# Kernel tuning notes

Hardware: AMD Instinct MI355X
Metric: run time of the kernel (lower is better)

Reference implementation:

```python
import jax, jax.numpy as jnp
import numpy as np
from jax import lax

H = 64            # hidden size
NUM_LAYERS = 3
EMBED_LEN = 128
B, T = 256, 2048


def _lstm_layer(x, Wih, Whh, bih, bhh):
    """x: [B, T, in]; returns full hidden sequence [B, T, H].
    PyTorch gate order: i, f, g, o."""
    Bn = x.shape[0]
    b = bih + bhh  # [4H]
    # Precompute input contribution for all timesteps: [T, B, 4H]
    xg = jnp.einsum('bti,gi->tbg', x, Wih) + b
    h0 = jnp.zeros((Bn, H), x.dtype)
    c0 = jnp.zeros((Bn, H), x.dtype)

    def step(carry, xg_t):
        h, c = carry
        gates = xg_t + h @ Whh.T  # [B, 4H]
        i, f, g, o = jnp.split(gates, 4, axis=-1)
        i = jax.nn.sigmoid(i)
        f = jax.nn.sigmoid(f)
        g = jnp.tanh(g)
        o = jax.nn.sigmoid(o)
        c = f * c + i * g
        h = o * jnp.tanh(c)
        return (h, c), h

    (_, _), hs = lax.scan(step, (h0, c0), xg)  # hs: [T, B, H]
    return jnp.swapaxes(hs, 0, 1)              # [B, T, H]


def setup_inputs() -> dict:
    key = jax.random.key(0)
    ks = jax.random.split(key, 20)
    k = 1.0 / np.sqrt(H)  # PyTorch default init bound

    def u(kk, shape):
        return jax.random.uniform(kk, shape, jnp.float32, -k, k)

    inp = {"x": jax.random.normal(ks[0], (B, 1, T), jnp.float32)}
    in_sizes = [1, H, H]
    idx = 1
    for l in range(NUM_LAYERS):
        inp[f"Wih{l}"] = u(ks[idx], (4 * H, in_sizes[l])); idx += 1
        inp[f"Whh{l}"] = u(ks[idx], (4 * H, H)); idx += 1
        inp[f"bih{l}"] = u(ks[idx], (4 * H,)); idx += 1
        inp[f"bhh{l}"] = u(ks[idx], (4 * H,)); idx += 1
    inp["fcW"] = u(ks[idx], (EMBED_LEN, H)); idx += 1
    inp["fcb"] = u(ks[idx], (EMBED_LEN,))
    return inp


def reference(x, Wih0, Whh0, bih0, bhh0,
              Wih1, Whh1, bih1, bhh1,
              Wih2, Whh2, bih2, bhh2,
              fcW, fcb):
    # forward: transpose [B,1,T] -> [B,T,1]
    h = jnp.swapaxes(x, 1, 2)
    h = _lstm_layer(h, Wih0, Whh0, bih0, bhh0)
    h = _lstm_layer(h, Wih1, Whh1, bih1, bhh1)
    h = _lstm_layer(h, Wih2, Whh2, bih2, bhh2)
    last = h[:, -1, :]              # [B, H]
    return last @ fcW.T + fcb       # [B, EMBED_LEN]
```

## Files before the change

kernel.cpp:

```cpp
#include <hip/hip_runtime.h>

#define T_LEN 2048
#define HID 64
#define EMB 128
#define WD 16
#define NWIN (T_LEN / WD)
#define NPH (NWIN + 4)

typedef _Float16 half2_t __attribute__((ext_vector_type(2)));
typedef unsigned uint4v __attribute__((ext_vector_type(4)));

#if __has_builtin(__builtin_amdgcn_exp2f)
#define EXP2F(x) __builtin_amdgcn_exp2f(x)
#else
#define EXP2F(x) exp2f(x)
#endif
#if __has_builtin(__builtin_amdgcn_rcpf)
#define RCPF(x) __builtin_amdgcn_rcpf(x)
#else
#define RCPF(x) (1.0f / (x))
#endif

#define LOG2E 1.4426950408889634f

__device__ __forceinline__ float fdot2(unsigned a, unsigned b, float c) {
    return __builtin_amdgcn_fdot2(__builtin_bit_cast(half2_t, a),
                                  __builtin_bit_cast(half2_t, b), c, false);
}

__device__ __forceinline__ float dotrow(const uint4v* w, const uint4v* g, float init) {
    float a0 = init, a1 = 0.f, a2 = 0.f, a3 = 0.f;
    #pragma unroll
    for (int q = 0; q < 8; ++q) {
        a0 = fdot2(w[q][0], g[q][0], a0);
        a1 = fdot2(w[q][1], g[q][1], a1);
        a2 = fdot2(w[q][2], g[q][2], a2);
        a3 = fdot2(w[q][3], g[q][3], a3);
    }
    return (a0 + a1) + (a2 + a3);
}

__device__ __forceinline__ uint4v pack8(float4 a, float4 b, float s) {
    half2_t h0{(_Float16)(a.x * s), (_Float16)(a.y * s)};
    half2_t h1{(_Float16)(a.z * s), (_Float16)(a.w * s)};
    half2_t h2{(_Float16)(b.x * s), (_Float16)(b.y * s)};
    half2_t h3{(_Float16)(b.z * s), (_Float16)(b.w * s)};
    uint4v q;
    q[0] = __builtin_bit_cast(unsigned, h0);
    q[1] = __builtin_bit_cast(unsigned, h1);
    q[2] = __builtin_bit_cast(unsigned, h2);
    q[3] = __builtin_bit_cast(unsigned, h3);
    return q;
}

__device__ __forceinline__ void cvt8(const float* __restrict__ Wp, float s, uint4v* dst) {
    const float4* p = reinterpret_cast<const float4*>(Wp);
    #pragma unroll
    for (int k = 0; k < 8; ++k) dst[k] = pack8(p[2 * k], p[2 * k + 1], s);
}

__global__ __launch_bounds__(512)
__attribute__((amdgpu_waves_per_eu(2, 2)))
void lstm3_fused(
    const float* __restrict__ x,
    const float* __restrict__ Wih0, const float* __restrict__ Whh0,
    const float* __restrict__ bih0, const float* __restrict__ bhh0,
    const float* __restrict__ Wih1, const float* __restrict__ Whh1,
    const float* __restrict__ bih1, const float* __restrict__ bhh1,
    const float* __restrict__ Wih2, const float* __restrict__ Whh2,
    const float* __restrict__ bih2, const float* __restrict__ bhh2,
    const float* __restrict__ fcW,  const float* __restrict__ fcb,
    float* __restrict__ out)
{
    const int b   = blockIdx.x;
    const int tid = threadIdx.x;
    const int wv  = tid >> 6;
    const int L   = tid & 63;

    __shared__ __align__(16) _Float16 h0ring[2 * WD][HID];
    __shared__ __align__(16) _Float16 h1ring[2 * WD][HID];
    __shared__ __align__(16) _Float16 h2ring[2][HID];
    __shared__ float p1buf[2][WD][4][HID];
    __shared__ float p2buf[2][WD][4][HID];
    __shared__ __align__(16) float xs[T_LEN];

    {
        const float4* xg4 = reinterpret_cast<const float4*>(x + b * T_LEN);
        reinterpret_cast<float4*>(xs)[tid] = xg4[tid];
        reinterpret_cast<unsigned*>(h0ring)[tid] = 0u;
        reinterpret_cast<unsigned*>(h0ring)[tid + 512] = 0u;
        reinterpret_cast<unsigned*>(h1ring)[tid] = 0u;
        reinterpret_cast<unsigned*>(h1ring)[tid + 512] = 0u;
        if (tid < 64) reinterpret_cast<unsigned*>(h2ring)[tid] = 0u;
    }

    const float sI = -LOG2E, sF = -LOG2E, sG = -2.f * LOG2E, sO = -LOG2E;
    const float scl[4] = {sI, sF, sG, sO};

    uint4v w[4][8];
    float bias4[4] = {0.f, 0.f, 0.f, 0.f};
    float wx4[4]   = {0.f, 0.f, 0.f, 0.f};

    if (wv < 3) {
        const float* Wh = (wv == 0) ? Whh0 : (wv == 1) ? Whh1 : Whh2;
        const float* bi = (wv == 0) ? bih0 : (wv == 1) ? bih1 : bih2;
        const float* bh = (wv == 0) ? bhh0 : (wv == 1) ? bhh1 : bhh2;
        #pragma unroll
        for (int c = 0; c < 4; ++c) {
            cvt8(Wh + (c * 64 + L) * 64, scl[c], w[c]);
            bias4[c] = (bi[c * 64 + L] + bh[c * 64 + L]) * scl[c];
        }
        if (wv == 0) {
            #pragma unroll
            for (int c = 0; c < 4; ++c) wx4[c] = Wih0[c * 64 + L] * scl[c];
        }
    } else if (wv == 4) {
        cvt8(Wih1 + (  0 + L) * 64, sI, w[0]);
    } else if (wv == 5) {
        cvt8(Wih1 + ( 64 + L) * 64, sF, w[0]);
    } else if (wv == 6) {
        cvt8(Wih1 + (128 + L) * 64, sG, w[0]);
    } else if (wv == 3) {
        cvt8(Wih1 + (192 + L) * 64, sO, w[0]);
        cvt8(Wih2 + (  0 + L) * 64, sI, w[1]);
    } else {
        cvt8(Wih2 + ( 64 + L) * 64, sF, w[0]);
        cvt8(Wih2 + (128 + L) * 64, sG, w[1]);
        cvt8(Wih2 + (192 + L) * 64, sO, w[2]);
    }

    float cst = 0.f;
    __syncthreads();

    for (int ph = 0; ph < NPH; ++ph) {
        const int par = ph & 1;

        if (wv == 0) {
            if (ph < NWIN) {
                _Float16* cur = &h0ring[par * WD][0];
                const _Float16* prv = &h0ring[(par ^ 1) * WD][0];
                const int tb = ph * WD;
                #pragma unroll 8
                for (int j = 0; j < WD; ++j) {
                    const uint4v* hp = reinterpret_cast<const uint4v*>(
                        (j == 0) ? (prv + (WD - 1) * HID) : (cur + (j - 1) * HID));
                    uint4v g[8];
                    #pragma unroll
                    for (int k = 0; k < 8; ++k) g[k] = hp[k];
                    float xv = xs[tb + j];
                    float d0 = dotrow(w[0], g, fmaf(wx4[0], xv, bias4[0]));
                    float d1 = dotrow(w[1], g, fmaf(wx4[1], xv, bias4[1]));
                    float d2 = dotrow(w[2], g, fmaf(wx4[2], xv, bias4[2]));
                    float d3 = dotrow(w[3], g, fmaf(wx4[3], xv, bias4[3]));
                    float ai = RCPF(1.f + EXP2F(d0));
                    float af = RCPF(1.f + EXP2F(d1));
                    float ag = fmaf(2.f, RCPF(1.f + EXP2F(d2)), -1.f);
                    float ao = RCPF(1.f + EXP2F(d3));
                    cst = fmaf(af, cst, ai * ag);
                    float tc = fmaf(2.f, RCPF(1.f + EXP2F(-2.f * LOG2E * cst)), -1.f);
                    cur[j * HID + L] = (_Float16)(ao * tc);
                }
            }
        } else if (wv == 1) {
            if (ph >= 2 && ph < NWIN + 2) {
                _Float16* cur = &h1ring[par * WD][0];
                const _Float16* prv = &h1ring[(par ^ 1) * WD][0];
                const float (*pb)[4][HID] = p1buf[par];
                #pragma unroll 8
                for (int j = 0; j < WD; ++j) {
                    const uint4v* hp = reinterpret_cast<const uint4v*>(
                        (j == 0) ? (prv + (WD - 1) * HID) : (cur + (j - 1) * HID));
                    uint4v g[8];
                    #pragma unroll
                    for (int k = 0; k < 8; ++k) g[k] = hp[k];
                    float d0 = dotrow(w[0], g, bias4[0] + pb[j][0][L]);
                    float d1 = dotrow(w[1], g, bias4[1] + pb[j][1][L]);
                    float d2 = dotrow(w[2], g, bias4[2] + pb[j][2][L]);
                    float d3 = dotrow(w[3], g, bias4[3] + pb[j][3][L]);
                    float ai = RCPF(1.f + EXP2F(d0));
                    float af = RCPF(1.f + EXP2F(d1));
                    float ag = fmaf(2.f, RCPF(1.f + EXP2F(d2)), -1.f);
                    float ao = RCPF(1.f + EXP2F(d3));
                    cst = fmaf(af, cst, ai * ag);
                    float tc = fmaf(2.f, RCPF(1.f + EXP2F(-2.f * LOG2E * cst)), -1.f);
                    cur[j * HID + L] = (_Float16)(ao * tc);
                }
            }
        } else if (wv == 2) {
            if (ph >= 4) {
                const float (*pb)[4][HID] = p2buf[par];
                #pragma unroll 8
                for (int j = 0; j < WD; ++j) {
                    const uint4v* hp = reinterpret_cast<const uint4v*>(
                        &h2ring[(j & 1) ^ 1][0]);
                    uint4v g[8];
                    #pragma unroll
                    for (int k = 0; k < 8; ++k) g[k] = hp[k];
                    float d0 = dotrow(w[0], g, bias4[0] + pb[j][0][L]);
                    float d1 = dotrow(w[1], g, bias4[1] + pb[j][1][L]);
                    float d2 = dotrow(w[2], g, bias4[2] + pb[j][2][L]);
                    float d3 = dotrow(w[3], g, bias4[3] + pb[j][3][L]);
                    float ai = RCPF(1.f + EXP2F(d0));
                    float af = RCPF(1.f + EXP2F(d1));
                    float ag = fmaf(2.f, RCPF(1.f + EXP2F(d2)), -1.f);
                    float ao = RCPF(1.f + EXP2F(d3));
                    cst = fmaf(af, cst, ai * ag);
                    float tc = fmaf(2.f, RCPF(1.f + EXP2F(-2.f * LOG2E * cst)), -1.f);
                    h2ring[j & 1][L] = (_Float16)(ao * tc);
                }
            }
        } else {
            const bool p1act = (ph >= 1 && ph < NWIN + 1);
            const bool p2act = (ph >= 3 && ph < NWIN + 3);
            if (wv == 4 || wv == 5 || wv == 6) {
                if (p1act) {
                    const _Float16* hw = &h0ring[(par ^ 1) * WD][0];
                    float (*po)[4][HID] = p1buf[par ^ 1];
                    const int c0 = wv - 4;
                    #pragma unroll 8
                    for (int j = 0; j < WD; ++j) {
                        const uint4v* hp = reinterpret_cast<const uint4v*>(hw + j * HID);
                        uint4v g[8];
                        #pragma unroll
                        for (int k = 0; k < 8; ++k) g[k] = hp[k];
                        po[j][c0][L] = dotrow(w[0], g, 0.f);
                    }
                }
            } else if (wv == 3) {
                if (p1act) {
                    const _Float16* hw = &h0ring[(par ^ 1) * WD][0];
                    float (*po)[4][HID] = p1buf[par ^ 1];
                    #pragma unroll 8
                    for (int j = 0; j < WD; ++j) {
                        const uint4v* hp = reinterpret_cast<const uint4v*>(hw + j * HID);
                        uint4v g[8];
                        #pragma unroll
                        for (int k = 0; k < 8; ++k) g[k] = hp[k];
                        po[j][3][L] = dotrow(w[0], g, 0.f);
                    }
                }
                if (p2act) {
                    const _Float16* hw = &h1ring[(par ^ 1) * WD][0];
                    float (*po)[4][HID] = p2buf[par ^ 1];
                    #pragma unroll 8
                    for (int j = 0; j < WD; ++j) {
                        const uint4v* hp = reinterpret_cast<const uint4v*>(hw + j * HID);
                        uint4v g[8];
                        #pragma unroll
                        for (int k = 0; k < 8; ++k) g[k] = hp[k];
                        po[j][0][L] = dotrow(w[1], g, 0.f);
                    }
                }
            } else {
                if (p2act) {
                    const _Float16* hw = &h1ring[(par ^ 1) * WD][0];
                    float (*po)[4][HID] = p2buf[par ^ 1];
                    #pragma unroll 4
                    for (int j = 0; j < WD; ++j) {
                        const uint4v* hp = reinterpret_cast<const uint4v*>(hw + j * HID);
                        uint4v g[8];
                        #pragma unroll
                        for (int k = 0; k < 8; ++k) g[k] = hp[k];
                        po[j][1][L] = dotrow(w[0], g, 0.f);
                        po[j][2][L] = dotrow(w[1], g, 0.f);
                        po[j][3][L] = dotrow(w[2], g, 0.f);
                    }
                }
            }
        }

        __syncthreads();
    }

    if (tid < EMB) {
        float acc = fcb[tid];
        const _Float16* hf = &h2ring[1][0];
        const float4* W4 = reinterpret_cast<const float4*>(fcW + tid * HID);
        #pragma unroll
        for (int k = 0; k < 16; ++k) {
            float4 wv4 = W4[k];
            acc = fmaf(wv4.x, (float)hf[4 * k + 0], acc);
            acc = fmaf(wv4.y, (float)hf[4 * k + 1], acc);
            acc = fmaf(wv4.z, (float)hf[4 * k + 2], acc);
            acc = fmaf(wv4.w, (float)hf[4 * k + 3], acc);
        }
        out[b * EMB + tid] = acc;
    }
}

extern "C" void kernel_launch(void* const* d_in, const int* in_sizes, int n_in,
                              void* d_out, int out_size, void* d_ws, size_t ws_size,
                              hipStream_t stream) {
    const float* x    = (const float*)d_in[0];
    const float* Wih0 = (const float*)d_in[1];
    const float* Whh0 = (const float*)d_in[2];
    const float* bih0 = (const float*)d_in[3];
    const float* bhh0 = (const float*)d_in[4];
    const float* Wih1 = (const float*)d_in[5];
    const float* Whh1 = (const float*)d_in[6];
    const float* bih1 = (const float*)d_in[7];
    const float* bhh1 = (const float*)d_in[8];
    const float* Wih2 = (const float*)d_in[9];
    const float* Whh2 = (const float*)d_in[10];
    const float* bih2 = (const float*)d_in[11];
    const float* bhh2 = (const float*)d_in[12];
    const float* fcW  = (const float*)d_in[13];
    const float* fcb  = (const float*)d_in[14];
    float* out = (float*)d_out;

    lstm3_fused<<<dim3(256), dim3(512), 0, stream>>>(
        x, Wih0, Whh0, bih0, bhh0,
        Wih1, Whh1, bih1, bhh1,
        Wih2, Whh2, bih2, bhh2,
        fcW, fcb, out);
}
```

Measured before the change: 1.085 ms.

## Replace per-phase block barrier with per-wave LDS flag dependencies and halve window

```diff
diff --git a/kernel.cpp b/kernel.cpp
--- a/kernel.cpp
+++ b/kernel.cpp
@@ -3,7 +3,7 @@
 #define T_LEN 2048
 #define HID 64
 #define EMB 128
-#define WD 16
+#define WD 8
 #define NWIN (T_LEN / WD)
 #define NPH (NWIN + 4)
 
@@ -57,6 +57,10 @@
     const float4* p = reinterpret_cast<const float4*>(Wp);
     #pragma unroll
     for (int k = 0; k < 8; ++k) dst[k] = pack8(p[2 * k], p[2 * k + 1], s);
+}
+
+__device__ __forceinline__ int ldf(int* f) {
+    return __hip_atomic_load(f, __ATOMIC_RELAXED, __HIP_MEMORY_SCOPE_WORKGROUP);
 }
 
 __global__ __launch_bounds__(512)
@@ -83,15 +87,15 @@
     __shared__ float p1buf[2][WD][4][HID];
     __shared__ float p2buf[2][WD][4][HID];
     __shared__ __align__(16) float xs[T_LEN];
+    __shared__ int flags[8];
 
     {
         const float4* xg4 = reinterpret_cast<const float4*>(x + b * T_LEN);
         reinterpret_cast<float4*>(xs)[tid] = xg4[tid];
-        reinterpret_cast<unsigned*>(h0ring)[tid] = 0u;
-        reinterpret_cast<unsigned*>(h0ring)[tid + 512] = 0u;
-        reinterpret_cast<unsigned*>(h1ring)[tid] = 0u;
-        reinterpret_cast<unsigned*>(h1ring)[tid + 512] = 0u;
+        reinterpret_cast<unsigned*>(h0ring)[tid & 511] = 0u;
+        reinterpret_cast<unsigned*>(h1ring)[tid & 511] = 0u;
         if (tid < 64) reinterpret_cast<unsigned*>(h2ring)[tid] = 0u;
+        if (tid < 8) flags[tid] = 0;
     }
 
     const float sI = -LOG2E, sF = -LOG2E, sG = -2.f * LOG2E, sO = -LOG2E;
@@ -135,12 +139,36 @@
     for (int ph = 0; ph < NPH; ++ph) {
         const int par = ph & 1;
 
+        {
+            bool ok;
+            do {
+                if (wv == 0)
+                    ok = (ldf(&flags[3]) >= ph) & (ldf(&flags[4]) >= ph)
+                       & (ldf(&flags[5]) >= ph) & (ldf(&flags[6]) >= ph);
+                else if (wv == 1)
+                    ok = (ldf(&flags[3]) >= ph) & (ldf(&flags[4]) >= ph)
+                       & (ldf(&flags[5]) >= ph) & (ldf(&flags[6]) >= ph)
+                       & (ldf(&flags[7]) >= ph);
+                else if (wv == 2)
+                    ok = (ldf(&flags[3]) >= ph) & (ldf(&flags[7]) >= ph);
+                else if (wv == 3)
+                    ok = (ldf(&flags[0]) >= ph) & (ldf(&flags[1]) >= ph)
+                       & (ldf(&flags[2]) >= ph);
+                else if (wv == 7)
+                    ok = (ldf(&flags[1]) >= ph) & (ldf(&flags[2]) >= ph);
+                else
+                    ok = (ldf(&flags[0]) >= ph) & (ldf(&flags[1]) >= ph);
+                if (!ok) __builtin_amdgcn_s_sleep(1);
+            } while (!ok);
+            __builtin_amdgcn_fence(__ATOMIC_ACQUIRE, "workgroup");
+        }
+
         if (wv == 0) {
             if (ph < NWIN) {
                 _Float16* cur = &h0ring[par * WD][0];
                 const _Float16* prv = &h0ring[(par ^ 1) * WD][0];
                 const int tb = ph * WD;
-                #pragma unroll 8
+                #pragma unroll
                 for (int j = 0; j < WD; ++j) {
                     const uint4v* hp = reinterpret_cast<const uint4v*>(
                         (j == 0) ? (prv + (WD - 1) * HID) : (cur + (j - 1) * HID));
@@ -166,7 +194,7 @@
                 _Float16* cur = &h1ring[par * WD][0];
                 const _Float16* prv = &h1ring[(par ^ 1) * WD][0];
                 const float (*pb)[4][HID] = p1buf[par];
-                #pragma unroll 8
+                #pragma unroll
                 for (int j = 0; j < WD; ++j) {
                     const uint4v* hp = reinterpret_cast<const uint4v*>(
                         (j == 0) ? (prv + (WD - 1) * HID) : (cur + (j - 1) * HID));
@@ -189,7 +217,7 @@
         } else if (wv == 2) {
             if (ph >= 4) {
                 const float (*pb)[4][HID] = p2buf[par];
-                #pragma unroll 8
+                #pragma unroll
                 for (int j = 0; j < WD; ++j) {
                     const uint4v* hp = reinterpret_cast<const uint4v*>(
                         &h2ring[(j & 1) ^ 1][0]);
@@ -217,7 +245,7 @@
                     const _Float16* hw = &h0ring[(par ^ 1) * WD][0];
                     float (*po)[4][HID] = p1buf[par ^ 1];
                     const int c0 = wv - 4;
-                    #pragma unroll 8
+                    #pragma unroll
                     for (int j = 0; j < WD; ++j) {
                         const uint4v* hp = reinterpret_cast<const uint4v*>(hw + j * HID);
                         uint4v g[8];
@@ -230,7 +258,7 @@
                 if (p1act) {
                     const _Float16* hw = &h0ring[(par ^ 1) * WD][0];
                     float (*po)[4][HID] = p1buf[par ^ 1];
-                    #pragma unroll 8
+                    #pragma unroll
                     for (int j = 0; j < WD; ++j) {
                         const uint4v* hp = reinterpret_cast<const uint4v*>(hw + j * HID);
                         uint4v g[8];
@@ -242,7 +270,7 @@
                 if (p2act) {
                     const _Float16* hw = &h1ring[(par ^ 1) * WD][0];
                     float (*po)[4][HID] = p2buf[par ^ 1];
-                    #pragma unroll 8
+                    #pragma unroll
                     for (int j = 0; j < WD; ++j) {
                         const uint4v* hp = reinterpret_cast<const uint4v*>(hw + j * HID);
                         uint4v g[8];
@@ -255,7 +283,7 @@
                 if (p2act) {
                     const _Float16* hw = &h1ring[(par ^ 1) * WD][0];
                     float (*po)[4][HID] = p2buf[par ^ 1];
-                    #pragma unroll 4
+                    #pragma unroll
                     for (int j = 0; j < WD; ++j) {
                         const uint4v* hp = reinterpret_cast<const uint4v*>(hw + j * HID);
                         uint4v g[8];
@@ -269,8 +297,13 @@
             }
         }
 
-        __syncthreads();
-    }
+        __builtin_amdgcn_fence(__ATOMIC_RELEASE, "workgroup");
+        if ((tid & 63) == 0)
+            __hip_atomic_store(&flags[wv], ph + 1, __ATOMIC_RELAXED,
+                               __HIP_MEMORY_SCOPE_WORKGROUP);
+    }
+
+    __syncthreads();
 
     if (tid < EMB) {
         float acc = fcb[tid];
```

After: 1.027 ms. 5.4% less time.

## Grow block to 12 waves and split input projections across more waves

Applied to the files above, without the earlier changes.

```diff
diff --git a/kernel.cpp b/kernel.cpp
--- a/kernel.cpp
+++ b/kernel.cpp
@@ -3,7 +3,7 @@
 #define T_LEN 2048
 #define HID 64
 #define EMB 128
-#define WD 16
+#define WD 8
 #define NWIN (T_LEN / WD)
 #define NPH (NWIN + 4)
 
@@ -38,6 +38,18 @@
         a3 = fdot2(w[q][3], g[q][3], a3);
     }
     return (a0 + a1) + (a2 + a3);
+}
+
+__device__ __forceinline__ float dot16h(const uint4v* w, const uint4v* g) {
+    float e = 0.f, o = 0.f;
+    #pragma unroll
+    for (int q = 0; q < 4; ++q) {
+        e = fdot2(w[q][0], g[q][0], e);
+        o = fdot2(w[q][1], g[q][1], o);
+        e = fdot2(w[q][2], g[q][2], e);
+        o = fdot2(w[q][3], g[q][3], o);
+    }
+    return e + o;
 }
 
 __device__ __forceinline__ uint4v pack8(float4 a, float4 b, float s) {
@@ -58,9 +70,14 @@
     #pragma unroll
     for (int k = 0; k < 8; ++k) dst[k] = pack8(p[2 * k], p[2 * k + 1], s);
 }
-
-__global__ __launch_bounds__(512)
-__attribute__((amdgpu_waves_per_eu(2, 2)))
+__device__ __forceinline__ void cvt4(const float* __restrict__ Wp, float s, uint4v* dst) {
+    const float4* p = reinterpret_cast<const float4*>(Wp);
+    #pragma unroll
+    for (int k = 0; k < 4; ++k) dst[k] = pack8(p[2 * k], p[2 * k + 1], s);
+}
+
+__global__ __launch_bounds__(768)
+__attribute__((amdgpu_waves_per_eu(3, 3)))
 void lstm3_fused(
     const float* __restrict__ x,
     const float* __restrict__ Wih0, const float* __restrict__ Whh0,
@@ -80,18 +97,21 @@
     __shared__ __align__(16) _Float16 h0ring[2 * WD][HID];
     __shared__ __align__(16) _Float16 h1ring[2 * WD][HID];
     __shared__ __align__(16) _Float16 h2ring[2][HID];
-    __shared__ float p1buf[2][WD][4][HID];
+    __shared__ float p1a[2][WD][4][HID];
+    __shared__ float p1b[2][WD][4][HID];
     __shared__ float p2buf[2][WD][4][HID];
     __shared__ __align__(16) float xs[T_LEN];
 
     {
         const float4* xg4 = reinterpret_cast<const float4*>(x + b * T_LEN);
-        reinterpret_cast<float4*>(xs)[tid] = xg4[tid];
-        reinterpret_cast<unsigned*>(h0ring)[tid] = 0u;
-        reinterpret_cast<unsigned*>(h0ring)[tid + 512] = 0u;
-        reinterpret_cast<unsigned*>(h1ring)[tid] = 0u;
-        reinterpret_cast<unsigned*>(h1ring)[tid + 512] = 0u;
+        if (tid < 512) {
+            reinterpret_cast<float4*>(xs)[tid] = xg4[tid];
+            reinterpret_cast<unsigned*>(h0ring)[tid] = 0u;
+            reinterpret_cast<unsigned*>(h1ring)[tid] = 0u;
+        }
         if (tid < 64) reinterpret_cast<unsigned*>(h2ring)[tid] = 0u;
+        float* pz = &p1b[0][0][0][0];
+        for (int i = tid; i < 2 * WD * 4 * HID; i += 768) pz[i] = 0.f;
     }
 
     const float sI = -LOG2E, sF = -LOG2E, sG = -2.f * LOG2E, sO = -LOG2E;
@@ -114,19 +134,20 @@
             #pragma unroll
             for (int c = 0; c < 4; ++c) wx4[c] = Wih0[c * 64 + L] * scl[c];
         }
-    } else if (wv == 4) {
-        cvt8(Wih1 + (  0 + L) * 64, sI, w[0]);
-    } else if (wv == 5) {
-        cvt8(Wih1 + ( 64 + L) * 64, sF, w[0]);
-    } else if (wv == 6) {
-        cvt8(Wih1 + (128 + L) * 64, sG, w[0]);
+    } else if (wv == 4 || wv == 5 || wv == 6) {
+        const int c = wv - 4;
+        cvt4(Wih1 + (c * 64 + L) * 64, scl[c], w[0]);
+    } else if (wv == 8 || wv == 9 || wv == 10) {
+        const int c = wv - 8;
+        cvt4(Wih1 + (c * 64 + L) * 64 + 32, scl[c], w[0]);
     } else if (wv == 3) {
         cvt8(Wih1 + (192 + L) * 64, sO, w[0]);
         cvt8(Wih2 + (  0 + L) * 64, sI, w[1]);
-    } else {
+    } else if (wv == 7) {
         cvt8(Wih2 + ( 64 + L) * 64, sF, w[0]);
         cvt8(Wih2 + (128 + L) * 64, sG, w[1]);
-        cvt8(Wih2 + (192 + L) * 64, sO, w[2]);
+    } else {
+        cvt8(Wih2 + (192 + L) * 64, sO, w[0]);
     }
 
     float cst = 0.f;
@@ -140,7 +161,7 @@
                 _Float16* cur = &h0ring[par * WD][0];
                 const _Float16* prv = &h0ring[(par ^ 1) * WD][0];
                 const int tb = ph * WD;
-                #pragma unroll 8
+                #pragma unroll
                 for (int j = 0; j < WD; ++j) {
                     const uint4v* hp = reinterpret_cast<const uint4v*>(
                         (j == 0) ? (prv + (WD - 1) * HID) : (cur + (j - 1) * HID));
@@ -165,18 +186,19 @@
             if (ph >= 2 && ph < NWIN + 2) {
                 _Float16* cur = &h1ring[par * WD][0];
                 const _Float16* prv = &h1ring[(par ^ 1) * WD][0];
-                const float (*pb)[4][HID] = p1buf[par];
-                #pragma unroll 8
+                const float (*pa)[4][HID] = p1a[par];
+                const float (*pb)[4][HID] = p1b[par];
+                #pragma unroll
                 for (int j = 0; j < WD; ++j) {
                     const uint4v* hp = reinterpret_cast<const uint4v*>(
                         (j == 0) ? (prv + (WD - 1) * HID) : (cur + (j - 1) * HID));
                     uint4v g[8];
                     #pragma unroll
                     for (int k = 0; k < 8; ++k) g[k] = hp[k];
-                    float d0 = dotrow(w[0], g, bias4[0] + pb[j][0][L]);
-                    float d1 = dotrow(w[1], g, bias4[1] + pb[j][1][L]);
-                    float d2 = dotrow(w[2], g, bias4[2] + pb[j][2][L]);
-                    float d3 = dotrow(w[3], g, bias4[3] + pb[j][3][L]);
+                    float d0 = dotrow(w[0], g, bias4[0] + pa[j][0][L] + pb[j][0][L]);
+                    float d1 = dotrow(w[1], g, bias4[1] + pa[j][1][L] + pb[j][1][L]);
+                    float d2 = dotrow(w[2], g, bias4[2] + pa[j][2][L] + pb[j][2][L]);
+                    float d3 = dotrow(w[3], g, bias4[3] + pa[j][3][L] + pb[j][3][L]);
                     float ai = RCPF(1.f + EXP2F(d0));
                     float af = RCPF(1.f + EXP2F(d1));
                     float ag = fmaf(2.f, RCPF(1.f + EXP2F(d2)), -1.f);
@@ -189,7 +211,7 @@
         } else if (wv == 2) {
             if (ph >= 4) {
                 const float (*pb)[4][HID] = p2buf[par];
-                #pragma unroll 8
+                #pragma unroll
                 for (int j = 0; j < WD; ++j) {
                     const uint4v* hp = reinterpret_cast<const uint4v*>(
                         &h2ring[(j & 1) ^ 1][0]);
@@ -215,22 +237,36 @@
             if (wv == 4 || wv == 5 || wv == 6) {
                 if (p1act) {
                     const _Float16* hw = &h0ring[(par ^ 1) * WD][0];
-                    float (*po)[4][HID] = p1buf[par ^ 1];
-                    const int c0 = wv - 4;
-                    #pragma unroll 8
-                    for (int j = 0; j < WD; ++j) {
-                        const uint4v* hp = reinterpret_cast<const uint4v*>(hw + j * HID);
-                        uint4v g[8];
-                        #pragma unroll
-                        for (int k = 0; k < 8; ++k) g[k] = hp[k];
-                        po[j][c0][L] = dotrow(w[0], g, 0.f);
+                    float (*po)[4][HID] = p1a[par ^ 1];
+                    const int c = wv - 4;
+                    #pragma unroll
+                    for (int j = 0; j < WD; ++j) {
+                        const uint4v* hp = reinterpret_cast<const uint4v*>(hw + j * HID);
+                        uint4v g[4];
+                        #pragma unroll
+                        for (int k = 0; k < 4; ++k) g[k] = hp[k];
+                        po[j][c][L] = dot16h(w[0], g);
+                    }
+                }
+            } else if (wv == 8 || wv == 9 || wv == 10) {
+                if (p1act) {
+                    const _Float16* hw = &h0ring[(par ^ 1) * WD][0];
+                    float (*po)[4][HID] = p1b[par ^ 1];
+                    const int c = wv - 8;
+                    #pragma unroll
+                    for (int j = 0; j < WD; ++j) {
+                        const uint4v* hp = reinterpret_cast<const uint4v*>(hw + j * HID) + 4;
+                        uint4v g[4];
+                        #pragma unroll
+                        for (int k = 0; k < 4; ++k) g[k] = hp[k];
+                        po[j][c][L] = dot16h(w[0], g);
                     }
                 }
             } else if (wv == 3) {
                 if (p1act) {
                     const _Float16* hw = &h0ring[(par ^ 1) * WD][0];
-                    float (*po)[4][HID] = p1buf[par ^ 1];
-                    #pragma unroll 8
+                    float (*po)[4][HID] = p1a[par ^ 1];
+                    #pragma unroll
                     for (int j = 0; j < WD; ++j) {
                         const uint4v* hp = reinterpret_cast<const uint4v*>(hw + j * HID);
                         uint4v g[8];
@@ -242,28 +278,40 @@
                 if (p2act) {
                     const _Float16* hw = &h1ring[(par ^ 1) * WD][0];
                     float (*po)[4][HID] = p2buf[par ^ 1];
-                    #pragma unroll 8
+                    #pragma unroll
                     for (int j = 0; j < WD; ++j) {
                         const uint4v* hp = reinterpret_cast<const uint4v*>(hw + j * HID);
                         uint4v g[8];
                         #pragma unroll
                         for (int k = 0; k < 8; ++k) g[k] = hp[k];
                         po[j][0][L] = dotrow(w[1], g, 0.f);
+                    }
+                }
+            } else if (wv == 7) {
+                if (p2act) {
+                    const _Float16* hw = &h1ring[(par ^ 1) * WD][0];
+                    float (*po)[4][HID] = p2buf[par ^ 1];
+                    #pragma unroll
+                    for (int j = 0; j < WD; ++j) {
+                        const uint4v* hp = reinterpret_cast<const uint4v*>(hw + j * HID);
+                        uint4v g[8];
+                        #pragma unroll
+                        for (int k = 0; k < 8; ++k) g[k] = hp[k];
+                        po[j][1][L] = dotrow(w[0], g, 0.f);
+                        po[j][2][L] = dotrow(w[1], g, 0.f);
                     }
                 }
             } else {
                 if (p2act) {
                     const _Float16* hw = &h1ring[(par ^ 1) * WD][0];
                     float (*po)[4][HID] = p2buf[par ^ 1];
-                    #pragma unroll 4
+                    #pragma unroll
                     for (int j = 0; j < WD; ++j) {
                         const uint4v* hp = reinterpret_cast<const uint4v*>(hw + j * HID);
                         uint4v g[8];
                         #pragma unroll
                         for (int k = 0; k < 8; ++k) g[k] = hp[k];
-                        po[j][1][L] = dotrow(w[0], g, 0.f);
-                        po[j][2][L] = dotrow(w[1], g, 0.f);
-                        po[j][3][L] = dotrow(w[2], g, 0.f);
+                        po[j][3][L] = dotrow(w[0], g, 0.f);
                     }
                 }
             }
@@ -308,7 +356,7 @@
     const float* fcb  = (const float*)d_in[14];
     float* out = (float*)d_out;
 
-    lstm3_fused<<<dim3(256), dim3(512), 0, stream>>>(
+    lstm3_fused<<<dim3(256), dim3(768), 0, stream>>>(
         x, Wih0, Whh0, bih0, bhh0,
         Wih1, Whh1, bih1, bhh1,
         Wih2, Whh2, bih2, bhh2,
```

New measurement: 2.058 ms. 1.9x slower.

## Interleave gate preactivation buffers and halve the pipeline window width

Applied to the files above, without the earlier changes.

```diff
diff --git a/kernel.cpp b/kernel.cpp
--- a/kernel.cpp
+++ b/kernel.cpp
@@ -3,7 +3,7 @@
 #define T_LEN 2048
 #define HID 64
 #define EMB 128
-#define WD 16
+#define WD 8
 #define NWIN (T_LEN / WD)
 #define NPH (NWIN + 4)
 
@@ -80,17 +80,15 @@
     __shared__ __align__(16) _Float16 h0ring[2 * WD][HID];
     __shared__ __align__(16) _Float16 h1ring[2 * WD][HID];
     __shared__ __align__(16) _Float16 h2ring[2][HID];
-    __shared__ float p1buf[2][WD][4][HID];
-    __shared__ float p2buf[2][WD][4][HID];
+    __shared__ __align__(16) float p1buf[2][WD][4 * HID];
+    __shared__ __align__(16) float p2buf[2][WD][4 * HID];
     __shared__ __align__(16) float xs[T_LEN];
 
     {
         const float4* xg4 = reinterpret_cast<const float4*>(x + b * T_LEN);
         reinterpret_cast<float4*>(xs)[tid] = xg4[tid];
         reinterpret_cast<unsigned*>(h0ring)[tid] = 0u;
-        reinterpret_cast<unsigned*>(h0ring)[tid + 512] = 0u;
         reinterpret_cast<unsigned*>(h1ring)[tid] = 0u;
-        reinterpret_cast<unsigned*>(h1ring)[tid + 512] = 0u;
         if (tid < 64) reinterpret_cast<unsigned*>(h2ring)[tid] = 0u;
     }
 
@@ -140,7 +138,7 @@
                 _Float16* cur = &h0ring[par * WD][0];
                 const _Float16* prv = &h0ring[(par ^ 1) * WD][0];
                 const int tb = ph * WD;
-                #pragma unroll 8
+                #pragma unroll
                 for (int j = 0; j < WD; ++j) {
                     const uint4v* hp = reinterpret_cast<const uint4v*>(
                         (j == 0) ? (prv + (WD - 1) * HID) : (cur + (j - 1) * HID));
@@ -165,18 +163,19 @@
             if (ph >= 2 && ph < NWIN + 2) {
                 _Float16* cur = &h1ring[par * WD][0];
                 const _Float16* prv = &h1ring[(par ^ 1) * WD][0];
-                const float (*pb)[4][HID] = p1buf[par];
-                #pragma unroll 8
+                const float (*pb)[4 * HID] = p1buf[par];
+                #pragma unroll
                 for (int j = 0; j < WD; ++j) {
                     const uint4v* hp = reinterpret_cast<const uint4v*>(
                         (j == 0) ? (prv + (WD - 1) * HID) : (cur + (j - 1) * HID));
                     uint4v g[8];
                     #pragma unroll
                     for (int k = 0; k < 8; ++k) g[k] = hp[k];
-                    float d0 = dotrow(w[0], g, bias4[0] + pb[j][0][L]);
-                    float d1 = dotrow(w[1], g, bias4[1] + pb[j][1][L]);
-                    float d2 = dotrow(w[2], g, bias4[2] + pb[j][2][L]);
-                    float d3 = dotrow(w[3], g, bias4[3] + pb[j][3][L]);
+                    float4 pv = *reinterpret_cast<const float4*>(&pb[j][L * 4]);
+                    float d0 = dotrow(w[0], g, bias4[0] + pv.w);
+                    float d1 = dotrow(w[1], g, bias4[1] + pv.x);
+                    float d2 = dotrow(w[2], g, bias4[2] + pv.y);
+                    float d3 = dotrow(w[3], g, bias4[3] + pv.z);
                     float ai = RCPF(1.f + EXP2F(d0));
                     float af = RCPF(1.f + EXP2F(d1));
                     float ag = fmaf(2.f, RCPF(1.f + EXP2F(d2)), -1.f);
@@ -188,18 +187,19 @@
             }
         } else if (wv == 2) {
             if (ph >= 4) {
-                const float (*pb)[4][HID] = p2buf[par];
-                #pragma unroll 8
+                const float (*pb)[4 * HID] = p2buf[par];
+                #pragma unroll
                 for (int j = 0; j < WD; ++j) {
                     const uint4v* hp = reinterpret_cast<const uint4v*>(
                         &h2ring[(j & 1) ^ 1][0]);
                     uint4v g[8];
                     #pragma unroll
                     for (int k = 0; k < 8; ++k) g[k] = hp[k];
-                    float d0 = dotrow(w[0], g, bias4[0] + pb[j][0][L]);
-                    float d1 = dotrow(w[1], g, bias4[1] + pb[j][1][L]);
-                    float d2 = dotrow(w[2], g, bias4[2] + pb[j][2][L]);
-                    float d3 = dotrow(w[3], g, bias4[3] + pb[j][3][L]);
+                    float4 pv = *reinterpret_cast<const float4*>(&pb[j][L * 4]);
+                    float d0 = dotrow(w[0], g, bias4[0] + pv.w);
+                    float d1 = dotrow(w[1], g, bias4[1] + pv.x);
+                    float d2 = dotrow(w[2], g, bias4[2] + pv.y);
+                    float d3 = dotrow(w[3], g, bias4[3] + pv.z);
                     float ai = RCPF(1.f + EXP2F(d0));
                     float af = RCPF(1.f + EXP2F(d1));
                     float ag = fmaf(2.f, RCPF(1.f + EXP2F(d2)), -1.f);
@@ -215,55 +215,58 @@
             if (wv == 4 || wv == 5 || wv == 6) {
                 if (p1act) {
                     const _Float16* hw = &h0ring[(par ^ 1) * WD][0];
-                    float (*po)[4][HID] = p1buf[par ^ 1];
-                    const int c0 = wv - 4;
-                    #pragma unroll 8
+                    float (*po)[4 * HID] = p1buf[par ^ 1];
+                    const int pos = (wv == 4) ? 3 : (wv - 5);
+                    #pragma unroll
                     for (int j = 0; j < WD; ++j) {
                         const uint4v* hp = reinterpret_cast<const uint4v*>(hw + j * HID);
                         uint4v g[8];
                         #pragma unroll
                         for (int k = 0; k < 8; ++k) g[k] = hp[k];
-                        po[j][c0][L] = dotrow(w[0], g, 0.f);
+                        po[j][L * 4 + pos] = dotrow(w[0], g, 0.f);
                     }
                 }
             } else if (wv == 3) {
                 if (p1act) {
                     const _Float16* hw = &h0ring[(par ^ 1) * WD][0];
-                    float (*po)[4][HID] = p1buf[par ^ 1];
-                    #pragma unroll 8
+                    float (*po)[4 * HID] = p1buf[par ^ 1];
+                    #pragma unroll
                     for (int j = 0; j < WD; ++j) {
                         const uint4v* hp = reinterpret_cast<const uint4v*>(hw + j * HID);
                         uint4v g[8];
                         #pragma unroll
                         for (int k = 0; k < 8; ++k) g[k] = hp[k];
-                        po[j][3][L] = dotrow(w[0], g, 0.f);
+                        po[j][L * 4 + 2] = dotrow(w[0], g, 0.f);
                     }
                 }
                 if (p2act) {
                     const _Float16* hw = &h1ring[(par ^ 1) * WD][0];
-                    float (*po)[4][HID] = p2buf[par ^ 1];
-                    #pragma unroll 8
+                    float (*po)[4 * HID] = p2buf[par ^ 1];
+                    #pragma unroll
                     for (int j = 0; j < WD; ++j) {
                         const uint4v* hp = reinterpret_cast<const uint4v*>(hw + j * HID);
                         uint4v g[8];
                         #pragma unroll
                         for (int k = 0; k < 8; ++k) g[k] = hp[k];
-                        po[j][0][L] = dotrow(w[1], g, 0.f);
+                        po[j][L * 4 + 3] = dotrow(w[1], g, 0.f);
                     }
                 }
             } else {
                 if (p2act) {
                     const _Float16* hw = &h1ring[(par ^ 1) * WD][0];
-                    float (*po)[4][HID] = p2buf[par ^ 1];
-                    #pragma unroll 4
+                    float (*po)[4 * HID] = p2buf[par ^ 1];
+                    #pragma unroll
                     for (int j = 0; j < WD; ++j) {
                         const uint4v* hp = reinterpret_cast<const uint4v*>(hw + j * HID);
                         uint4v g[8];
                         #pragma unroll
                         for (int k = 0; k < 8; ++k) g[k] = hp[k];
-                        po[j][1][L] = dotrow(w[0], g, 0.f);
-                        po[j][2][L] = dotrow(w[1], g, 0.f);
-                        po[j][3][L] = dotrow(w[2], g, 0.f);
+                        float pf = dotrow(w[0], g, 0.f);
+                        float pg = dotrow(w[1], g, 0.f);
+                        float po3 = dotrow(w[2], g, 0.f);
+                        *reinterpret_cast<float2*>(&po[j][L * 4]) =
+                            make_float2(pf, pg);
+                        po[j][L * 4 + 2] = po3;
                     }
                 }
             }
```

Result: faster. 986.1 us (-9.1%).
